# Performance work log

Hardware: AMD Instinct MI355X
Metric: run time of the kernel (lower is better)

The kernel has to match this reference:

```python
import jax, jax.numpy as jnp
import numpy as np

SEQ_LEN = 12
BATCH = 2048
IN_DIM = 512
HIDDEN = 1024


def setup_inputs() -> dict:
    key = jax.random.key(0)
    k1, k2, k3, k4 = jax.random.split(key, 4)
    scale = 1.0 / np.sqrt(IN_DIM + HIDDEN)
    return {
        "x": jax.random.normal(k1, (BATCH, SEQ_LEN, IN_DIM), dtype=jnp.float32),
        "coded_cords": jax.random.normal(k2, (BATCH, HIDDEN), dtype=jnp.float32),
        # TF GRUCell fused gate kernel: [in+hidden, 2*hidden] (reset, update), bias init 1.0
        "gate_kernel": jax.random.normal(k3, (IN_DIM + HIDDEN, 2 * HIDDEN), dtype=jnp.float32) * scale,
        "gate_bias": jnp.ones((2 * HIDDEN,), dtype=jnp.float32),
        # candidate kernel: [in+hidden, hidden], zero bias
        "cand_kernel": jax.random.normal(k4, (IN_DIM + HIDDEN, HIDDEN), dtype=jnp.float32) * scale,
        "cand_bias": jnp.zeros((HIDDEN,), dtype=jnp.float32),
    }


def reference(x, coded_cords, gate_kernel, gate_bias, cand_kernel, cand_bias):
    # GRU recurrence (tf.contrib.rnn.GRUCell math), initial state = coded_cords.
    def step(h, xt):
        # xt: [B, D], h: [B, H]
        gates = jax.nn.sigmoid(jnp.concatenate([xt, h], axis=-1) @ gate_kernel + gate_bias)
        r, u = jnp.split(gates, 2, axis=-1)  # reset, update gates [B, H]
        c = jnp.tanh(jnp.concatenate([xt, r * h], axis=-1) @ cand_kernel + cand_bias)
        h_new = u * h + (1.0 - u) * c
        return h_new, h_new

    xs = jnp.swapaxes(x, 0, 1)  # [T, B, D]
    _, ys = jax.lax.scan(step, coded_cords, xs)  # ys: [T, B, H]
    return jnp.swapaxes(ys, 0, 1)  # [B, T, H]
```

## Files before the change

kernel.cpp:

```cpp
#include <hip/hip_runtime.h>
#include <hip/hip_bf16.h>


#define T_SEQ 12
#define BATCH 2048
#define IND 512
#define HID 1024
#define NGATE (2 * HID)
#define NPRE (NGATE + HID)

typedef __bf16 bf16x8 __attribute__((ext_vector_type(8)));
typedef __bf16 bf16x4 __attribute__((ext_vector_type(4)));
typedef float floatx4 __attribute__((ext_vector_type(4)));

#define AS1 __attribute__((address_space(1)))
#define AS3 __attribute__((address_space(3)))

__device__ __forceinline__ void gload16(const __bf16* g, __bf16* l) {
  __builtin_amdgcn_global_load_lds((const AS1 void*)g, (AS3 void*)l, 16, 0, 0);
}
__device__ __forceinline__ void gload16c(const __bf16* g, __bf16* l) {
  __builtin_amdgcn_global_load_lds((const AS1 void*)g, (AS3 void*)l, 16, 0, 1);
}

__device__ __forceinline__ float fast_sigmoid(float v) {
  v = fminf(30.f, fmaxf(-30.f, v));
  return 1.f / (1.f + __expf(-v));
}
__device__ __forceinline__ float fast_tanh(float v) {
  v = fminf(15.f, fmaxf(-15.f, v));
  float e = __expf(2.f * v);
  return (e - 1.f) / (e + 1.f);
}

__global__ __launch_bounds__(256) void prep(
    const float* __restrict__ Wg, const float* __restrict__ Wc,
    const float* __restrict__ x, const float* __restrict__ coded,
    __bf16* __restrict__ Bx, __bf16* __restrict__ Bhg, __bf16* __restrict__ Bhc,
    __bf16* __restrict__ xb, float* __restrict__ h32, __bf16* __restrict__ hb,
    unsigned* __restrict__ ctr) {
  int b = blockIdx.x;
  if (b < 2304) {
    int gid = b * 256 + threadIdx.x;
    int g = gid >> 6, lane = gid & 63;
    const float* W; int ld, row0, ksteps, wid; __bf16* out;
    if (g < 2048)      { W = Wg; ld = NGATE; row0 = 0;   ksteps = 16; wid = g;        out = Bx; }
    else if (g < 3072) { W = Wc; ld = HID;   row0 = 0;   ksteps = 16; wid = g - 2048; out = Bx + (size_t)2048 * 512; }
    else if (g < 7168) { W = Wg; ld = NGATE; row0 = IND; ksteps = 32; wid = g - 3072; out = Bhg; }
    else               { W = Wc; ld = HID;   row0 = IND; ksteps = 32; wid = g - 7168; out = Bhc; }
    int n16 = wid / ksteps, kt = wid - n16 * ksteps;
    int col = n16 * 16 + (lane & 15);
    int k0 = row0 + kt * 32 + (lane >> 4) * 8;
    bf16x8 v;
#pragma unroll
    for (int j = 0; j < 8; ++j) v[j] = (__bf16)W[(size_t)(k0 + j) * ld + col];
    *reinterpret_cast<bf16x8*>(out + (size_t)wid * 512 + lane * 8) = v;
  } else if (b < 4352) {
    int i = (b - 2304) * 256 + threadIdx.x;
    const float4* x4 = (const float4*)x;
    const int n4 = BATCH * T_SEQ * IND / 4;
    for (int k = i; k < n4; k += 2048 * 256) {
      float4 v = x4[k];
      bf16x4 o;
      o[0] = (__bf16)v.x; o[1] = (__bf16)v.y; o[2] = (__bf16)v.z; o[3] = (__bf16)v.w;
      *reinterpret_cast<bf16x4*>(xb + (size_t)k * 4) = o;
    }
  } else {
    int i = (b - 4352) * 256 + threadIdx.x;
    if (b == 4352) {
#pragma unroll
      for (int j = 0; j < 4; ++j) ctr[threadIdx.x + j * 256] = 0u;
    }
    float4 v = ((const float4*)coded)[i];
    ((float4*)h32)[i] = v;
    bf16x4 o;
    o[0] = (__bf16)v.x; o[1] = (__bf16)v.y; o[2] = (__bf16)v.z; o[3] = (__bf16)v.w;
    *reinterpret_cast<bf16x4*>(hb + (size_t)i * 4) = o;
  }
}

__global__ __launch_bounds__(256) void pre_gemm(
    const __bf16* __restrict__ xb, const __bf16* __restrict__ Bx,
    const float* __restrict__ bg, const float* __restrict__ bc,
    __bf16* __restrict__ Pg, __bf16* __restrict__ Pc) {
  __shared__ __bf16 Alds[128 * 64];
  __shared__ __bf16 Blds[8192];
  const int tid = threadIdx.x, lane = tid & 63, w = tid >> 6;
  const int wm = w >> 1, wn = w & 1, quad = lane >> 4, l16 = lane & 15;
  const int bid = blockIdx.x;
  const int wg = (bid & 7) * 576 + (bid >> 3);
  const int nb = wg % 24;
  const int rest = wg / 24;
  const int mB = rest & 15;
  const int tz = rest >> 4;
  const int m0 = mB * 128;

  const __bf16* gA[4]; __bf16* lA[4];
  const __bf16* gB[4]; __bf16* lB[4];
#pragma unroll
  for (int i = 0; i < 4; ++i) {
    int c = tid + i * 256;
    int row = c >> 3, k8 = c & 7;
    gA[i] = xb + ((size_t)(m0 + row) * T_SEQ + tz) * IND + ((k8 ^ (row & 7)) * 8);
    lA[i] = Alds + c * 8;
    int ks2c = c >> 9, rem = c & 511;
    gB[i] = Bx + (((size_t)(nb * 8 + (rem >> 6)) * 16 + ks2c) * 64 + (rem & 63)) * 8;
    lB[i] = Blds + c * 8;
  }

  floatx4 acc[4][4] = {};
  for (int it = 0; it < 8; ++it) {
    __syncthreads();
#pragma unroll
    for (int i = 0; i < 4; ++i) gload16(gA[i] + it * 64, lA[i]);
#pragma unroll
    for (int i = 0; i < 4; ++i) gload16(gB[i] + (size_t)it * 1024, lB[i]);
    __syncthreads();
#pragma unroll
    for (int ks2 = 0; ks2 < 2; ++ks2) {
      bf16x8 af[4], bfr[4];
#pragma unroll
      for (int mf = 0; mf < 4; ++mf) {
        int row = wm * 64 + mf * 16 + l16;
        af[mf] = *(const bf16x8*)&Alds[row * 64 + (((ks2 * 4 + quad) ^ (row & 7)) * 8)];
      }
#pragma unroll
      for (int nf = 0; nf < 4; ++nf)
        bfr[nf] = *(const bf16x8*)&Blds[(ks2 * 512 + (wn * 4 + nf) * 64 + lane) * 8];
#pragma unroll
      for (int mf = 0; mf < 4; ++mf)
#pragma unroll
        for (int nf = 0; nf < 4; ++nf)
          acc[mf][nf] = __builtin_amdgcn_mfma_f32_16x16x32_bf16(af[mf], bfr[nf], acc[mf][nf], 0, 0, 0);
    }
  }

  const int n64g = nb * 2 + wn;
  const bool isg = (n64g < 32);
  __bf16* P = isg ? Pg : Pc;
  const float* bias = isg ? bg : bc;
  const int nrel = isg ? n64g : (n64g - 32);
  const int colb = nrel * 64 + l16;
#pragma unroll
  for (int mf = 0; mf < 4; ++mf) {
    int m32 = mB * 4 + wm * 2 + (mf >> 1);
    size_t tb = isg ? (((size_t)tz * 64 + m32) * 32 + n64g) * 2048
                    : (((size_t)tz * 64 + m32) * 16 + nrel) * 2048;
#pragma unroll
    for (int nf = 0; nf < 4; ++nf) {
      float bv = bias[colb + nf * 16];
      bf16x4 st;
#pragma unroll
      for (int i = 0; i < 4; ++i) st[i] = (__bf16)(acc[mf][nf][i] + bv);
      *(bf16x4*)&P[tb + (size_t)(((mf & 1) * 4 + nf) * 64 + lane) * 4] = st;
    }
  }
}

__global__ __launch_bounds__(256, 2) void gru_steps(
    const __bf16* __restrict__ Bhg, const __bf16* __restrict__ Bhc,
    const __bf16* __restrict__ Pg, const __bf16* __restrict__ Pc,
    float* __restrict__ h32, __bf16* __restrict__ hb,
    __bf16* __restrict__ rhb, float* __restrict__ out,
    unsigned* __restrict__ ctr) {
  __shared__ __bf16 Alds[64 * 128];
  __shared__ __bf16 Blds[16384];
  float* uS = (float*)&Blds[8192];
  const int tid = threadIdx.x, lane = tid & 63, w = tid >> 6;
  const int wm = w >> 1, wn = w & 1, quad = lane >> 4, l16 = lane & 15;
  const int bid = blockIdx.x;
  const int mT = (bid & 7) * 4 + ((bid >> 3) & 3);
  const int sub = bid >> 5;
  unsigned* cG = ctr + mT * 16;
  unsigned* cC = ctr + 512 + mT * 16;

  int offA[4];
#pragma unroll
  for (int i = 0; i < 4; ++i) {
    int c = tid + i * 256, row = c >> 4, ch = c & 15;
    offA[i] = (mT * 64 + row) * HID + ((ch ^ (row & 7)) * 8);
  }

  for (int t = 0; t < T_SEQ; ++t) {
    {
      floatx4 acc[2][4] = {};
      __bf16 hr[2][4][4];
      for (int kt = 0; kt < 8; ++kt) {
        __syncthreads();
#pragma unroll
        for (int i = 0; i < 4; ++i)
          gload16c(hb + offA[i] + kt * 128, Alds + (tid + i * 256) * 8);
#pragma unroll
        for (int i = 0; i < 8; ++i) {
          int gidx = (i < 4) ? (sub * 4 + i) : (64 + sub * 4 + (i - 4));
          gload16(Bhg + (size_t)gidx * 16384 + kt * 2048 + tid * 8,
                  Blds + (tid + i * 256) * 8);
        }
        __syncthreads();
#pragma unroll
        for (int ks2 = 0; ks2 < 4; ++ks2) {
          bf16x8 af[2], bfr[4];
#pragma unroll
          for (int mf = 0; mf < 2; ++mf) {
            int row = wm * 32 + mf * 16 + l16;
            af[mf] = *(const bf16x8*)&Alds[row * 128 + (((ks2 * 4 + quad) ^ (row & 7)) * 8)];
          }
#pragma unroll
          for (int nf = 0; nf < 4; ++nf)
            bfr[nf] = *(const bf16x8*)&Blds[(wn * 4 + nf) * 2048 + ks2 * 512 + lane * 8];
#pragma unroll
          for (int mf = 0; mf < 2; ++mf)
#pragma unroll
            for (int nf = 0; nf < 4; ++nf)
              acc[mf][nf] = __builtin_amdgcn_mfma_f32_16x16x32_bf16(af[mf], bfr[nf], acc[mf][nf], 0, 0, 0);
        }
        if (kt == (sub >> 1) && wn == 0) {
#pragma unroll
          for (int mf = 0; mf < 2; ++mf)
#pragma unroll
            for (int nf = 0; nf < 4; ++nf)
#pragma unroll
              for (int i = 0; i < 4; ++i) {
                int r = wm * 32 + mf * 16 + quad * 4 + i;
                int c = (sub & 1) * 64 + nf * 16 + l16;
                hr[mf][nf][i] = Alds[r * 128 + (((c >> 3) ^ (r & 7)) * 8) + (c & 7)];
              }
        }
      }
      const int n64 = wn * 16 + sub;
      const int m32 = mT * 2 + wm;
      size_t tb = (((size_t)t * 64 + m32) * 32 + n64) * 2048;
#pragma unroll
      for (int mf = 0; mf < 2; ++mf)
#pragma unroll
        for (int nf = 0; nf < 4; ++nf) {
          bf16x4 px = *(const bf16x4*)&Pg[tb + (size_t)((mf * 4 + nf) * 64 + lane) * 4];
          int rowb = mT * 64 + wm * 32 + mf * 16 + quad * 4;
#pragma unroll
          for (int i = 0; i < 4; ++i) {
            float s = fast_sigmoid(acc[mf][nf][i] + (float)px[i]);
            if (wn == 0) {
              rhb[(size_t)(rowb + i) * HID + sub * 64 + nf * 16 + l16] =
                  (__bf16)(s * (float)hr[mf][nf][i]);
            } else {
              uS[(wm * 32 + mf * 16 + quad * 4 + i) * 64 + nf * 16 + l16] = s;
            }
          }
        }
    }
    __syncthreads();
    if (tid == 0) {
      __hip_atomic_fetch_add(cG, 1u, __ATOMIC_RELAXED, __HIP_MEMORY_SCOPE_AGENT);
      unsigned tgt = 16u * (t + 1);
      while (__hip_atomic_load(cG, __ATOMIC_RELAXED, __HIP_MEMORY_SCOPE_AGENT) < tgt)
        __builtin_amdgcn_s_sleep(2);
    }
    __syncthreads();
    {
      floatx4 acc[2][2] = {};
      for (int kt = 0; kt < 8; ++kt) {
        __syncthreads();
#pragma unroll
        for (int i = 0; i < 4; ++i)
          gload16c(rhb + offA[i] + kt * 128, Alds + (tid + i * 256) * 8);
#pragma unroll
        for (int i = 0; i < 4; ++i)
          gload16(Bhc + (size_t)(sub * 4 + i) * 16384 + kt * 2048 + tid * 8,
                  Blds + (tid + i * 256) * 8);
        __syncthreads();
#pragma unroll
        for (int ks2 = 0; ks2 < 4; ++ks2) {
          bf16x8 af[2], bfr[2];
#pragma unroll
          for (int mf = 0; mf < 2; ++mf) {
            int row = wm * 32 + mf * 16 + l16;
            af[mf] = *(const bf16x8*)&Alds[row * 128 + (((ks2 * 4 + quad) ^ (row & 7)) * 8)];
          }
#pragma unroll
          for (int nf = 0; nf < 2; ++nf)
            bfr[nf] = *(const bf16x8*)&Blds[(wn * 2 + nf) * 2048 + ks2 * 512 + lane * 8];
#pragma unroll
          for (int mf = 0; mf < 2; ++mf)
#pragma unroll
            for (int nf = 0; nf < 2; ++nf)
              acc[mf][nf] = __builtin_amdgcn_mfma_f32_16x16x32_bf16(af[mf], bfr[nf], acc[mf][nf], 0, 0, 0);
        }
      }
      const int m32 = mT * 2 + wm;
      size_t tb = (((size_t)t * 64 + m32) * 16 + sub) * 2048;
#pragma unroll
      for (int mf = 0; mf < 2; ++mf)
#pragma unroll
        for (int nf = 0; nf < 2; ++nf) {
          bf16x4 px = *(const bf16x4*)&Pc[tb + (size_t)((mf * 4 + wn * 2 + nf) * 64 + lane) * 4];
          int col = sub * 64 + wn * 32 + nf * 16 + l16;
          int rowb = mT * 64 + wm * 32 + mf * 16 + quad * 4;
#pragma unroll
          for (int i = 0; i < 4; ++i) {
            float c = fast_tanh(acc[mf][nf][i] + (float)px[i]);
            size_t idx = (size_t)(rowb + i) * HID + col;
            float u = uS[(wm * 32 + mf * 16 + quad * 4 + i) * 64 + wn * 32 + nf * 16 + l16];
            float hnew = u * h32[idx] + (1.f - u) * c;
            h32[idx] = hnew;
            hb[idx] = (__bf16)hnew;
            __builtin_nontemporal_store(hnew, &out[(size_t)(rowb + i) * (T_SEQ * HID) + t * HID + col]);
          }
        }
    }
    __syncthreads();
    if (tid == 0) {
      __hip_atomic_fetch_add(cC, 1u, __ATOMIC_RELAXED, __HIP_MEMORY_SCOPE_AGENT);
      unsigned tgt = 16u * (t + 1);
      while (__hip_atomic_load(cC, __ATOMIC_RELAXED, __HIP_MEMORY_SCOPE_AGENT) < tgt)
        __builtin_amdgcn_s_sleep(2);
    }
    __syncthreads();
  }
}

extern "C" void kernel_launch(void* const* d_in, const int* in_sizes, int n_in,
                              void* d_out, int out_size, void* d_ws, size_t ws_size,
                              hipStream_t stream) {
  const float* x     = (const float*)d_in[0];
  const float* coded = (const float*)d_in[1];
  const float* Wg_f  = (const float*)d_in[2];
  const float* bg    = (const float*)d_in[3];
  const float* Wc_f  = (const float*)d_in[4];
  const float* bc    = (const float*)d_in[5];
  float* out = (float*)d_out;

  uintptr_t base = ((uintptr_t)d_ws + 255) & ~(uintptr_t)255;
  auto take = [&](size_t bytes) {
    void* p = (void*)base;
    base = (base + bytes + 255) & ~(uintptr_t)255;
    return p;
  };
  __bf16* Bx  = (__bf16*)take((size_t)(NPRE / 16) * 16 * 512 * 2);
  __bf16* Bhg = (__bf16*)take((size_t)(NGATE / 16) * 32 * 512 * 2);
  __bf16* Bhc = (__bf16*)take((size_t)(HID / 16) * 32 * 512 * 2);
  __bf16* Pg  = (__bf16*)take((size_t)T_SEQ * 64 * 32 * 2048 * 2);
  __bf16* Pc  = (__bf16*)take((size_t)T_SEQ * 64 * 16 * 2048 * 2);
  __bf16* xb  = (__bf16*)take((size_t)BATCH * T_SEQ * IND * 2);
  float*  h32 = (float*) take((size_t)BATCH * HID * 4);
  __bf16* hb  = (__bf16*)take((size_t)BATCH * HID * 2);
  __bf16* rhb = (__bf16*)take((size_t)BATCH * HID * 2);
  unsigned* ctr = (unsigned*)take(1024 * sizeof(unsigned));

  prep<<<6400, 256, 0, stream>>>(Wg_f, Wc_f, x, coded, Bx, Bhg, Bhc, xb, h32, hb, ctr);

  pre_gemm<<<4608, 256, 0, stream>>>(xb, Bx, bg, bc, Pg, Pc);

  gru_steps<<<512, 256, 0, stream>>>(Bhg, Bhc, Pg, Pc, h32, hb, rhb, out, ctr);
}
```

Measured before the change: 716.8 us.

## Fuse input projection GEMM into recurrent GRU step kernel

Removes the separate pre_gemm kernel and its Pg/Pc bf16 buffers. Each step's gate and candidate GEMMs now run four extra K-tiles over the x slice and Bx weights before the hidden-state tiles, and add the biases directly. This saves the large precomputed-projection write and read traffic and one kernel launch. In exchange, the x-projection work moves onto the serial recurrent critical path, which runs with only 512 blocks. It also swizzles the uS shared buffer to avoid bank conflicts and reads h for r*h from global instead of caching it from LDS.

```diff
diff --git a/kernel.cpp b/kernel.cpp
--- a/kernel.cpp
+++ b/kernel.cpp
@@ -79,87 +79,10 @@
   }
 }
 
-__global__ __launch_bounds__(256) void pre_gemm(
-    const __bf16* __restrict__ xb, const __bf16* __restrict__ Bx,
+__global__ __launch_bounds__(256, 2) void gru_steps(
+    const __bf16* __restrict__ Bx, const __bf16* __restrict__ Bhg,
+    const __bf16* __restrict__ Bhc, const __bf16* __restrict__ xb,
     const float* __restrict__ bg, const float* __restrict__ bc,
-    __bf16* __restrict__ Pg, __bf16* __restrict__ Pc) {
-  __shared__ __bf16 Alds[128 * 64];
-  __shared__ __bf16 Blds[8192];
-  const int tid = threadIdx.x, lane = tid & 63, w = tid >> 6;
-  const int wm = w >> 1, wn = w & 1, quad = lane >> 4, l16 = lane & 15;
-  const int bid = blockIdx.x;
-  const int wg = (bid & 7) * 576 + (bid >> 3);
-  const int nb = wg % 24;
-  const int rest = wg / 24;
-  const int mB = rest & 15;
-  const int tz = rest >> 4;
-  const int m0 = mB * 128;
-
-  const __bf16* gA[4]; __bf16* lA[4];
-  const __bf16* gB[4]; __bf16* lB[4];
-#pragma unroll
-  for (int i = 0; i < 4; ++i) {
-    int c = tid + i * 256;
-    int row = c >> 3, k8 = c & 7;
-    gA[i] = xb + ((size_t)(m0 + row) * T_SEQ + tz) * IND + ((k8 ^ (row & 7)) * 8);
-    lA[i] = Alds + c * 8;
-    int ks2c = c >> 9, rem = c & 511;
-    gB[i] = Bx + (((size_t)(nb * 8 + (rem >> 6)) * 16 + ks2c) * 64 + (rem & 63)) * 8;
-    lB[i] = Blds + c * 8;
-  }
-
-  floatx4 acc[4][4] = {};
-  for (int it = 0; it < 8; ++it) {
-    __syncthreads();
-#pragma unroll
-    for (int i = 0; i < 4; ++i) gload16(gA[i] + it * 64, lA[i]);
-#pragma unroll
-    for (int i = 0; i < 4; ++i) gload16(gB[i] + (size_t)it * 1024, lB[i]);
-    __syncthreads();
-#pragma unroll
-    for (int ks2 = 0; ks2 < 2; ++ks2) {
-      bf16x8 af[4], bfr[4];
-#pragma unroll
-      for (int mf = 0; mf < 4; ++mf) {
-        int row = wm * 64 + mf * 16 + l16;
-        af[mf] = *(const bf16x8*)&Alds[row * 64 + (((ks2 * 4 + quad) ^ (row & 7)) * 8)];
-      }
-#pragma unroll
-      for (int nf = 0; nf < 4; ++nf)
-        bfr[nf] = *(const bf16x8*)&Blds[(ks2 * 512 + (wn * 4 + nf) * 64 + lane) * 8];
-#pragma unroll
-      for (int mf = 0; mf < 4; ++mf)
-#pragma unroll
-        for (int nf = 0; nf < 4; ++nf)
-          acc[mf][nf] = __builtin_amdgcn_mfma_f32_16x16x32_bf16(af[mf], bfr[nf], acc[mf][nf], 0, 0, 0);
-    }
-  }
-
-  const int n64g = nb * 2 + wn;
-  const bool isg = (n64g < 32);
-  __bf16* P = isg ? Pg : Pc;
-  const float* bias = isg ? bg : bc;
-  const int nrel = isg ? n64g : (n64g - 32);
-  const int colb = nrel * 64 + l16;
-#pragma unroll
-  for (int mf = 0; mf < 4; ++mf) {
-    int m32 = mB * 4 + wm * 2 + (mf >> 1);
-    size_t tb = isg ? (((size_t)tz * 64 + m32) * 32 + n64g) * 2048
-                    : (((size_t)tz * 64 + m32) * 16 + nrel) * 2048;
-#pragma unroll
-    for (int nf = 0; nf < 4; ++nf) {
-      float bv = bias[colb + nf * 16];
-      bf16x4 st;
-#pragma unroll
-      for (int i = 0; i < 4; ++i) st[i] = (__bf16)(acc[mf][nf][i] + bv);
-      *(bf16x4*)&P[tb + (size_t)(((mf & 1) * 4 + nf) * 64 + lane) * 4] = st;
-    }
-  }
-}
-
-__global__ __launch_bounds__(256, 2) void gru_steps(
-    const __bf16* __restrict__ Bhg, const __bf16* __restrict__ Bhc,
-    const __bf16* __restrict__ Pg, const __bf16* __restrict__ Pc,
     float* __restrict__ h32, __bf16* __restrict__ hb,
     __bf16* __restrict__ rhb, float* __restrict__ out,
     unsigned* __restrict__ ctr) {
@@ -174,27 +97,49 @@
   unsigned* cG = ctr + mT * 16;
   unsigned* cC = ctr + 512 + mT * 16;
 
-  int offA[4];
+  auto uSi = [](int r, int c) { return r * 64 + (c ^ (((r >> 2) & 3) << 4)); };
+
+  int axOff[4], ahOff[4];
 #pragma unroll
   for (int i = 0; i < 4; ++i) {
-    int c = tid + i * 256, row = c >> 4, ch = c & 15;
-    offA[i] = (mT * 64 + row) * HID + ((ch ^ (row & 7)) * 8);
+    int c = tid + i * 256, row = c >> 4, x8 = ((c & 15) ^ (row & 7)) * 8;
+    axOff[i] = (mT * 64 + row) * (T_SEQ * IND) + x8;
+    ahOff[i] = (mT * 64 + row) * HID + x8;
+  }
+  int bgx[8], bgh[8], bcx[4], bch[4];
+#pragma unroll
+  for (int i = 0; i < 8; ++i) {
+    int n16g = (i < 4) ? (sub * 4 + i) : (64 + sub * 4 + (i - 4));
+    bgx[i] = n16g * 8192 + tid * 8;
+    bgh[i] = n16g * 16384 + tid * 8;
+  }
+#pragma unroll
+  for (int i = 0; i < 4; ++i) {
+    int n16c = sub * 4 + i;
+    bcx[i] = 2048 * 512 + n16c * 8192 + tid * 8;
+    bch[i] = n16c * 16384 + tid * 8;
   }
 
   for (int t = 0; t < T_SEQ; ++t) {
+    const int xT = t * 512;
     {
       floatx4 acc[2][4] = {};
-      __bf16 hr[2][4][4];
-      for (int kt = 0; kt < 8; ++kt) {
-        __syncthreads();
-#pragma unroll
-        for (int i = 0; i < 4; ++i)
-          gload16c(hb + offA[i] + kt * 128, Alds + (tid + i * 256) * 8);
-#pragma unroll
-        for (int i = 0; i < 8; ++i) {
-          int gidx = (i < 4) ? (sub * 4 + i) : (64 + sub * 4 + (i - 4));
-          gload16(Bhg + (size_t)gidx * 16384 + kt * 2048 + tid * 8,
-                  Blds + (tid + i * 256) * 8);
+      for (int kt = 0; kt < 12; ++kt) {
+        __syncthreads();
+        if (kt < 4) {
+#pragma unroll
+          for (int i = 0; i < 4; ++i)
+            gload16(xb + axOff[i] + xT + kt * 128, Alds + (tid + i * 256) * 8);
+#pragma unroll
+          for (int i = 0; i < 8; ++i)
+            gload16(Bx + bgx[i] + kt * 2048, Blds + (tid + i * 256) * 8);
+        } else {
+#pragma unroll
+          for (int i = 0; i < 4; ++i)
+            gload16c(hb + ahOff[i] + (kt - 4) * 128, Alds + (tid + i * 256) * 8);
+#pragma unroll
+          for (int i = 0; i < 8; ++i)
+            gload16(Bhg + bgh[i] + (kt - 4) * 2048, Blds + (tid + i * 256) * 8);
         }
         __syncthreads();
 #pragma unroll
@@ -214,39 +159,28 @@
             for (int nf = 0; nf < 4; ++nf)
               acc[mf][nf] = __builtin_amdgcn_mfma_f32_16x16x32_bf16(af[mf], bfr[nf], acc[mf][nf], 0, 0, 0);
         }
-        if (kt == (sub >> 1) && wn == 0) {
-#pragma unroll
-          for (int mf = 0; mf < 2; ++mf)
-#pragma unroll
-            for (int nf = 0; nf < 4; ++nf)
-#pragma unroll
-              for (int i = 0; i < 4; ++i) {
-                int r = wm * 32 + mf * 16 + quad * 4 + i;
-                int c = (sub & 1) * 64 + nf * 16 + l16;
-                hr[mf][nf][i] = Alds[r * 128 + (((c >> 3) ^ (r & 7)) * 8) + (c & 7)];
-              }
-        }
-      }
-      const int n64 = wn * 16 + sub;
-      const int m32 = mT * 2 + wm;
-      size_t tb = (((size_t)t * 64 + m32) * 32 + n64) * 2048;
-#pragma unroll
-      for (int mf = 0; mf < 2; ++mf)
+      }
+      const int colb = (wn * 16 + sub) * 64 + l16;
+      float bgv[4];
+#pragma unroll
+      for (int nf = 0; nf < 4; ++nf) bgv[nf] = bg[colb + nf * 16];
+#pragma unroll
+      for (int mf = 0; mf < 2; ++mf) {
+        int rowb = mT * 64 + wm * 32 + mf * 16 + quad * 4;
 #pragma unroll
         for (int nf = 0; nf < 4; ++nf) {
-          bf16x4 px = *(const bf16x4*)&Pg[tb + (size_t)((mf * 4 + nf) * 64 + lane) * 4];
-          int rowb = mT * 64 + wm * 32 + mf * 16 + quad * 4;
 #pragma unroll
           for (int i = 0; i < 4; ++i) {
-            float s = fast_sigmoid(acc[mf][nf][i] + (float)px[i]);
+            float s = fast_sigmoid(acc[mf][nf][i] + bgv[nf]);
             if (wn == 0) {
-              rhb[(size_t)(rowb + i) * HID + sub * 64 + nf * 16 + l16] =
-                  (__bf16)(s * (float)hr[mf][nf][i]);
+              size_t idx = (size_t)(rowb + i) * HID + sub * 64 + nf * 16 + l16;
+              rhb[idx] = (__bf16)(s * (float)hb[idx]);
             } else {
-              uS[(wm * 32 + mf * 16 + quad * 4 + i) * 64 + nf * 16 + l16] = s;
+              uS[uSi(wm * 32 + mf * 16 + quad * 4 + i, nf * 16 + l16)] = s;
             }
           }
         }
+      }
     }
     __syncthreads();
     if (tid == 0) {
@@ -258,15 +192,23 @@
     __syncthreads();
     {
       floatx4 acc[2][2] = {};
-      for (int kt = 0; kt < 8; ++kt) {
-        __syncthreads();
-#pragma unroll
-        for (int i = 0; i < 4; ++i)
-          gload16c(rhb + offA[i] + kt * 128, Alds + (tid + i * 256) * 8);
-#pragma unroll
-        for (int i = 0; i < 4; ++i)
-          gload16(Bhc + (size_t)(sub * 4 + i) * 16384 + kt * 2048 + tid * 8,
-                  Blds + (tid + i * 256) * 8);
+      for (int kt = 0; kt < 12; ++kt) {
+        __syncthreads();
+        if (kt < 4) {
+#pragma unroll
+          for (int i = 0; i < 4; ++i)
+            gload16(xb + axOff[i] + xT + kt * 128, Alds + (tid + i * 256) * 8);
+#pragma unroll
+          for (int i = 0; i < 4; ++i)
+            gload16(Bx + bcx[i] + kt * 2048, Blds + (tid + i * 256) * 8);
+        } else {
+#pragma unroll
+          for (int i = 0; i < 4; ++i)
+            gload16c(rhb + ahOff[i] + (kt - 4) * 128, Alds + (tid + i * 256) * 8);
+#pragma unroll
+          for (int i = 0; i < 4; ++i)
+            gload16(Bhc + bch[i] + (kt - 4) * 2048, Blds + (tid + i * 256) * 8);
+        }
         __syncthreads();
 #pragma unroll
         for (int ks2 = 0; ks2 < 4; ++ks2) {
@@ -286,26 +228,25 @@
               acc[mf][nf] = __builtin_amdgcn_mfma_f32_16x16x32_bf16(af[mf], bfr[nf], acc[mf][nf], 0, 0, 0);
         }
       }
-      const int m32 = mT * 2 + wm;
-      size_t tb = (((size_t)t * 64 + m32) * 16 + sub) * 2048;
-#pragma unroll
-      for (int mf = 0; mf < 2; ++mf)
+#pragma unroll
+      for (int mf = 0; mf < 2; ++mf) {
 #pragma unroll
         for (int nf = 0; nf < 2; ++nf) {
-          bf16x4 px = *(const bf16x4*)&Pc[tb + (size_t)((mf * 4 + wn * 2 + nf) * 64 + lane) * 4];
           int col = sub * 64 + wn * 32 + nf * 16 + l16;
+          float bcv = bc[col];
           int rowb = mT * 64 + wm * 32 + mf * 16 + quad * 4;
 #pragma unroll
           for (int i = 0; i < 4; ++i) {
-            float c = fast_tanh(acc[mf][nf][i] + (float)px[i]);
+            float c = fast_tanh(acc[mf][nf][i] + bcv);
             size_t idx = (size_t)(rowb + i) * HID + col;
-            float u = uS[(wm * 32 + mf * 16 + quad * 4 + i) * 64 + wn * 32 + nf * 16 + l16];
+            float u = uS[uSi(wm * 32 + mf * 16 + quad * 4 + i, wn * 32 + nf * 16 + l16)];
             float hnew = u * h32[idx] + (1.f - u) * c;
             h32[idx] = hnew;
             hb[idx] = (__bf16)hnew;
             __builtin_nontemporal_store(hnew, &out[(size_t)(rowb + i) * (T_SEQ * HID) + t * HID + col]);
           }
         }
+      }
     }
     __syncthreads();
     if (tid == 0) {
@@ -338,8 +279,6 @@
   __bf16* Bx  = (__bf16*)take((size_t)(NPRE / 16) * 16 * 512 * 2);
   __bf16* Bhg = (__bf16*)take((size_t)(NGATE / 16) * 32 * 512 * 2);
   __bf16* Bhc = (__bf16*)take((size_t)(HID / 16) * 32 * 512 * 2);
-  __bf16* Pg  = (__bf16*)take((size_t)T_SEQ * 64 * 32 * 2048 * 2);
-  __bf16* Pc  = (__bf16*)take((size_t)T_SEQ * 64 * 16 * 2048 * 2);
   __bf16* xb  = (__bf16*)take((size_t)BATCH * T_SEQ * IND * 2);
   float*  h32 = (float*) take((size_t)BATCH * HID * 4);
   __bf16* hb  = (__bf16*)take((size_t)BATCH * HID * 2);
@@ -348,7 +287,5 @@
 
   prep<<<6400, 256, 0, stream>>>(Wg_f, Wc_f, x, coded, Bx, Bhg, Bhc, xb, h32, hb, ctr);
 
-  pre_gemm<<<4608, 256, 0, stream>>>(xb, Bx, bg, bc, Pg, Pc);
-
-  gru_steps<<<512, 256, 0, stream>>>(Bhg, Bhc, Pg, Pc, h32, hb, rhb, out, ctr);
-}
+  gru_steps<<<512, 256, 0, stream>>>(Bx, Bhg, Bhc, xb, bg, bc, h32, hb, rhb, out, ctr);
+}
```

After: 1.097 ms. +53.0%, slower.

## Halve GRU step tile rows and double persistent blocks for more occupancy

Applied to the files above, without the earlier changes.

The recurrent kernel now uses 32-row batch tiles instead of 64, launching 1024 persistent blocks with smaller LDS and a K-tile of 64, so more blocks fit per CU. Each wave now covers all rows and a slice of columns. The reset-gate multiply reads h from the fp32 state instead of caching it from LDS during the GEMM. The uS buffer gets its own swizzled LDS array, and the counter array is enlarged for the extra tiles. This buys more parallelism and latency hiding per step, at the cost of twice as many barrier groups and more redundant weight loads per block. It also relies on all 1024 blocks being co-resident, because of the spin barriers.

```diff
diff --git a/kernel.cpp b/kernel.cpp
--- a/kernel.cpp
+++ b/kernel.cpp
@@ -69,7 +69,7 @@
     int i = (b - 4352) * 256 + threadIdx.x;
     if (b == 4352) {
 #pragma unroll
-      for (int j = 0; j < 4; ++j) ctr[threadIdx.x + j * 256] = 0u;
+      for (int j = 0; j < 8; ++j) ctr[threadIdx.x + j * 256] = 0u;
     }
     float4 v = ((const float4*)coded)[i];
     ((float4*)h32)[i] = v;
@@ -157,96 +157,91 @@
   }
 }
 
-__global__ __launch_bounds__(256, 2) void gru_steps(
+__global__ __launch_bounds__(256, 5) void gru_steps(
     const __bf16* __restrict__ Bhg, const __bf16* __restrict__ Bhc,
     const __bf16* __restrict__ Pg, const __bf16* __restrict__ Pc,
     float* __restrict__ h32, __bf16* __restrict__ hb,
     __bf16* __restrict__ rhb, float* __restrict__ out,
     unsigned* __restrict__ ctr) {
-  __shared__ __bf16 Alds[64 * 128];
-  __shared__ __bf16 Blds[16384];
-  float* uS = (float*)&Blds[8192];
+  __shared__ __bf16 Alds[32 * 64];
+  __shared__ __bf16 Blds[8192];
+  __shared__ float uS[32 * 64];
   const int tid = threadIdx.x, lane = tid & 63, w = tid >> 6;
-  const int wm = w >> 1, wn = w & 1, quad = lane >> 4, l16 = lane & 15;
+  const int quad = lane >> 4, l16 = lane & 15;
   const int bid = blockIdx.x;
-  const int mT = (bid & 7) * 4 + ((bid >> 3) & 3);
-  const int sub = bid >> 5;
+  const int mT = (bid & 7) * 8 + ((bid >> 3) & 7);
+  const int sub = bid >> 6;
   unsigned* cG = ctr + mT * 16;
-  unsigned* cC = ctr + 512 + mT * 16;
-
-  int offA[4];
+  unsigned* cC = ctr + 1024 + mT * 16;
+
+  auto uSi = [](int r, int c) { return r * 64 + (c ^ (((r >> 2) & 3) << 4)); };
+
+  const int arow = tid >> 3;
+  const int ahOff = (mT * 32 + arow) * HID + (((tid & 7) ^ (arow & 7)) * 8);
+  int bghS[4], bchS[2];
 #pragma unroll
   for (int i = 0; i < 4; ++i) {
-    int c = tid + i * 256, row = c >> 4, ch = c & 15;
-    offA[i] = (mT * 64 + row) * HID + ((ch ^ (row & 7)) * 8);
+    int c = tid + i * 256, s = c >> 7;
+    int n16g = (s < 4) ? (sub * 4 + s) : (64 + sub * 4 + (s - 4));
+    bghS[i] = n16g * 16384 + (c & 127) * 8;
+  }
+#pragma unroll
+  for (int i = 0; i < 2; ++i) {
+    int c = tid + i * 256;
+    bchS[i] = (sub * 4 + (c >> 7)) * 16384 + (c & 127) * 8;
   }
 
   for (int t = 0; t < T_SEQ; ++t) {
     {
-      floatx4 acc[2][4] = {};
-      __bf16 hr[2][4][4];
-      for (int kt = 0; kt < 8; ++kt) {
+      floatx4 acc[2][2] = {};
+      for (int kt = 0; kt < 16; ++kt) {
         __syncthreads();
+        gload16c(hb + ahOff + kt * 64, Alds + tid * 8);
 #pragma unroll
         for (int i = 0; i < 4; ++i)
-          gload16c(hb + offA[i] + kt * 128, Alds + (tid + i * 256) * 8);
-#pragma unroll
-        for (int i = 0; i < 8; ++i) {
-          int gidx = (i < 4) ? (sub * 4 + i) : (64 + sub * 4 + (i - 4));
-          gload16(Bhg + (size_t)gidx * 16384 + kt * 2048 + tid * 8,
-                  Blds + (tid + i * 256) * 8);
-        }
+          gload16(Bhg + bghS[i] + kt * 1024, Blds + (tid + i * 256) * 8);
         __syncthreads();
 #pragma unroll
-        for (int ks2 = 0; ks2 < 4; ++ks2) {
-          bf16x8 af[2], bfr[4];
+        for (int ks2 = 0; ks2 < 2; ++ks2) {
+          bf16x8 af[2], bfr[2];
 #pragma unroll
           for (int mf = 0; mf < 2; ++mf) {
-            int row = wm * 32 + mf * 16 + l16;
-            af[mf] = *(const bf16x8*)&Alds[row * 128 + (((ks2 * 4 + quad) ^ (row & 7)) * 8)];
+            int row = mf * 16 + l16;
+            af[mf] = *(const bf16x8*)&Alds[row * 64 + (((ks2 * 4 + quad) ^ (row & 7)) * 8)];
           }
 #pragma unroll
-          for (int nf = 0; nf < 4; ++nf)
-            bfr[nf] = *(const bf16x8*)&Blds[(wn * 4 + nf) * 2048 + ks2 * 512 + lane * 8];
+          for (int nf = 0; nf < 2; ++nf)
+            bfr[nf] = *(const bf16x8*)&Blds[(w * 2 + nf) * 1024 + ks2 * 512 + lane * 8];
 #pragma unroll
           for (int mf = 0; mf < 2; ++mf)
 #pragma unroll
-            for (int nf = 0; nf < 4; ++nf)
+            for (int nf = 0; nf < 2; ++nf)
               acc[mf][nf] = __builtin_amdgcn_mfma_f32_16x16x32_bf16(af[mf], bfr[nf], acc[mf][nf], 0, 0, 0);
         }
-        if (kt == (sub >> 1) && wn == 0) {
-#pragma unroll
-          for (int mf = 0; mf < 2; ++mf)
-#pragma unroll
-            for (int nf = 0; nf < 4; ++nf)
-#pragma unroll
-              for (int i = 0; i < 4; ++i) {
-                int r = wm * 32 + mf * 16 + quad * 4 + i;
-                int c = (sub & 1) * 64 + nf * 16 + l16;
-                hr[mf][nf][i] = Alds[r * 128 + (((c >> 3) ^ (r & 7)) * 8) + (c & 7)];
-              }
-        }
-      }
-      const int n64 = wn * 16 + sub;
-      const int m32 = mT * 2 + wm;
-      size_t tb = (((size_t)t * 64 + m32) * 32 + n64) * 2048;
-#pragma unroll
-      for (int mf = 0; mf < 2; ++mf)
-#pragma unroll
-        for (int nf = 0; nf < 4; ++nf) {
-          bf16x4 px = *(const bf16x4*)&Pg[tb + (size_t)((mf * 4 + nf) * 64 + lane) * 4];
-          int rowb = mT * 64 + wm * 32 + mf * 16 + quad * 4;
+      }
+      const bool isr = (w < 2);
+      const int n64 = isr ? sub : (16 + sub);
+      size_t tb = (((size_t)t * 64 + mT) * 32 + n64) * 2048;
+#pragma unroll
+      for (int mf = 0; mf < 2; ++mf) {
+        int rowb = mT * 32 + mf * 16 + quad * 4;
+#pragma unroll
+        for (int nf = 0; nf < 2; ++nf) {
+          bf16x4 px = *(const bf16x4*)&Pg[tb + (size_t)((mf * 4 + (w & 1) * 2 + nf) * 64 + lane) * 4];
+          int cl = (w & 1) * 32 + nf * 16 + l16;
 #pragma unroll
           for (int i = 0; i < 4; ++i) {
             float s = fast_sigmoid(acc[mf][nf][i] + (float)px[i]);
-            if (wn == 0) {
-              rhb[(size_t)(rowb + i) * HID + sub * 64 + nf * 16 + l16] =
-                  (__bf16)(s * (float)hr[mf][nf][i]);
+            if (isr) {
+              size_t idx = (size_t)(rowb + i) * HID + sub * 64 + cl;
+              float hv = (float)(__bf16)h32[idx];
+              rhb[idx] = (__bf16)(s * hv);
             } else {
-              uS[(wm * 32 + mf * 16 + quad * 4 + i) * 64 + nf * 16 + l16] = s;
+              uS[uSi(mf * 16 + quad * 4 + i, cl)] = s;
             }
           }
         }
+      }
     }
     __syncthreads();
     if (tid == 0) {
@@ -257,55 +252,45 @@
     }
     __syncthreads();
     {
-      floatx4 acc[2][2] = {};
-      for (int kt = 0; kt < 8; ++kt) {
+      floatx4 acc2[2] = {};
+      for (int kt = 0; kt < 16; ++kt) {
         __syncthreads();
-#pragma unroll
-        for (int i = 0; i < 4; ++i)
-          gload16c(rhb + offA[i] + kt * 128, Alds + (tid + i * 256) * 8);
-#pragma unroll
-        for (int i = 0; i < 4; ++i)
-          gload16(Bhc + (size_t)(sub * 4 + i) * 16384 + kt * 2048 + tid * 8,
-                  Blds + (tid + i * 256) * 8);
+        gload16c(rhb + ahOff + kt * 64, Alds + tid * 8);
+#pragma unroll
+        for (int i = 0; i < 2; ++i)
+          gload16(Bhc + bchS[i] + kt * 1024, Blds + (tid + i * 256) * 8);
         __syncthreads();
 #pragma unroll
-        for (int ks2 = 0; ks2 < 4; ++ks2) {
-          bf16x8 af[2], bfr[2];
+        for (int ks2 = 0; ks2 < 2; ++ks2) {
+          bf16x8 af[2], bfr;
 #pragma unroll
           for (int mf = 0; mf < 2; ++mf) {
-            int row = wm * 32 + mf * 16 + l16;
-            af[mf] = *(const bf16x8*)&Alds[row * 128 + (((ks2 * 4 + quad) ^ (row & 7)) * 8)];
+            int row = mf * 16 + l16;
+            af[mf] = *(const bf16x8*)&Alds[row * 64 + (((ks2 * 4 + quad) ^ (row & 7)) * 8)];
           }
-#pragma unroll
-          for (int nf = 0; nf < 2; ++nf)
-            bfr[nf] = *(const bf16x8*)&Blds[(wn * 2 + nf) * 2048 + ks2 * 512 + lane * 8];
+          bfr = *(const bf16x8*)&Blds[w * 1024 + ks2 * 512 + lane * 8];
 #pragma unroll
           for (int mf = 0; mf < 2; ++mf)
-#pragma unroll
-            for (int nf = 0; nf < 2; ++nf)
-              acc[mf][nf] = __builtin_amdgcn_mfma_f32_16x16x32_bf16(af[mf], bfr[nf], acc[mf][nf], 0, 0, 0);
+            acc2[mf] = __builtin_amdgcn_mfma_f32_16x16x32_bf16(af[mf], bfr, acc2[mf], 0, 0, 0);
         }
       }
-      const int m32 = mT * 2 + wm;
-      size_t tb = (((size_t)t * 64 + m32) * 16 + sub) * 2048;
-#pragma unroll
-      for (int mf = 0; mf < 2; ++mf)
-#pragma unroll
-        for (int nf = 0; nf < 2; ++nf) {
-          bf16x4 px = *(const bf16x4*)&Pc[tb + (size_t)((mf * 4 + wn * 2 + nf) * 64 + lane) * 4];
-          int col = sub * 64 + wn * 32 + nf * 16 + l16;
-          int rowb = mT * 64 + wm * 32 + mf * 16 + quad * 4;
-#pragma unroll
-          for (int i = 0; i < 4; ++i) {
-            float c = fast_tanh(acc[mf][nf][i] + (float)px[i]);
-            size_t idx = (size_t)(rowb + i) * HID + col;
-            float u = uS[(wm * 32 + mf * 16 + quad * 4 + i) * 64 + wn * 32 + nf * 16 + l16];
-            float hnew = u * h32[idx] + (1.f - u) * c;
-            h32[idx] = hnew;
-            hb[idx] = (__bf16)hnew;
-            __builtin_nontemporal_store(hnew, &out[(size_t)(rowb + i) * (T_SEQ * HID) + t * HID + col]);
-          }
+      size_t tb = (((size_t)t * 64 + mT) * 16 + sub) * 2048;
+#pragma unroll
+      for (int mf = 0; mf < 2; ++mf) {
+        bf16x4 px = *(const bf16x4*)&Pc[tb + (size_t)((mf * 4 + w) * 64 + lane) * 4];
+        int col = sub * 64 + w * 16 + l16;
+        int rowb = mT * 32 + mf * 16 + quad * 4;
+#pragma unroll
+        for (int i = 0; i < 4; ++i) {
+          float c = fast_tanh(acc2[mf][i] + (float)px[i]);
+          size_t idx = (size_t)(rowb + i) * HID + col;
+          float u = uS[uSi(mf * 16 + quad * 4 + i, w * 16 + l16)];
+          float hnew = u * h32[idx] + (1.f - u) * c;
+          h32[idx] = hnew;
+          hb[idx] = (__bf16)hnew;
+          __builtin_nontemporal_store(hnew, &out[(size_t)(rowb + i) * (T_SEQ * HID) + t * HID + col]);
         }
+      }
     }
     __syncthreads();
     if (tid == 0) {
@@ -344,11 +329,11 @@
   float*  h32 = (float*) take((size_t)BATCH * HID * 4);
   __bf16* hb  = (__bf16*)take((size_t)BATCH * HID * 2);
   __bf16* rhb = (__bf16*)take((size_t)BATCH * HID * 2);
-  unsigned* ctr = (unsigned*)take(1024 * sizeof(unsigned));
+  unsigned* ctr = (unsigned*)take(2048 * sizeof(unsigned));
 
   prep<<<6400, 256, 0, stream>>>(Wg_f, Wc_f, x, coded, Bx, Bhg, Bhc, xb, h32, hb, ctr);
 
   pre_gemm<<<4608, 256, 0, stream>>>(xb, Bx, bg, bc, Pg, Pc);
 
-  gru_steps<<<512, 256, 0, stream>>>(Bhg, Bhc, Pg, Pc, h32, hb, rhb, out, ctr);
-}
+  gru_steps<<<1024, 256, 0, stream>>>(Bhg, Bhc, Pg, Pc, h32, hb, rhb, out, ctr);
+}
```

Result: slower. 1.149 ms (+60.3%).

## Double-buffer LDS tiles in GRU step GEMMs with halved K-tile

Applied to the files above, without the earlier changes.

Both recurrent GEMM phases in gru_steps now use two LDS buffers with a 64-wide K tile over 16 iterations. Loads for the next tile are issued before computing the current one, so there is one barrier per iteration instead of two. The reset-gate product now reads h from global h32, rounded to bf16, instead of capturing it from LDS. The update gate is stored as fp16 in a swizzled LDS region. This aims to hide global-to-LDS latency behind MFMA work, at the cost of extra global reads of h and twice as many loop iterations.

```diff
diff --git a/kernel.cpp b/kernel.cpp
--- a/kernel.cpp
+++ b/kernel.cpp
@@ -69,7 +69,7 @@
     int i = (b - 4352) * 256 + threadIdx.x;
     if (b == 4352) {
 #pragma unroll
-      for (int j = 0; j < 4; ++j) ctr[threadIdx.x + j * 256] = 0u;
+      for (int j = 0; j < 8; ++j) ctr[threadIdx.x + j * 256] = 0u;
     }
     float4 v = ((const float4*)coded)[i];
     ((float4*)h32)[i] = v;
@@ -163,9 +163,9 @@
     float* __restrict__ h32, __bf16* __restrict__ hb,
     __bf16* __restrict__ rhb, float* __restrict__ out,
     unsigned* __restrict__ ctr) {
-  __shared__ __bf16 Alds[64 * 128];
+  __shared__ __bf16 Alds[2][4096];
   __shared__ __bf16 Blds[16384];
-  float* uS = (float*)&Blds[8192];
+  _Float16* uS = (_Float16*)&Blds[12288];
   const int tid = threadIdx.x, lane = tid & 63, w = tid >> 6;
   const int wm = w >> 1, wn = w & 1, quad = lane >> 4, l16 = lane & 15;
   const int bid = blockIdx.x;
@@ -174,79 +174,87 @@
   unsigned* cG = ctr + mT * 16;
   unsigned* cC = ctr + 512 + mT * 16;
 
-  int offA[4];
+  auto uSi = [](int r, int c) { return r * 64 + (c ^ (((r >> 2) & 3) << 4)); };
+
+  int ahOff[2];
+#pragma unroll
+  for (int i = 0; i < 2; ++i) {
+    int c = tid + i * 256, row = c >> 3;
+    ahOff[i] = (mT * 64 + row) * HID + (((c & 7) ^ (row & 7)) * 8);
+  }
+  int bghS[4];
 #pragma unroll
   for (int i = 0; i < 4; ++i) {
-    int c = tid + i * 256, row = c >> 4, ch = c & 15;
-    offA[i] = (mT * 64 + row) * HID + ((ch ^ (row & 7)) * 8);
+    int c = tid + i * 256, s = c >> 7;
+    int n16g = (s < 4) ? (sub * 4 + s) : (64 + sub * 4 + (s - 4));
+    bghS[i] = n16g * 16384 + (c & 127) * 8;
+  }
+  int bchS[2];
+#pragma unroll
+  for (int i = 0; i < 2; ++i) {
+    int c = tid + i * 256;
+    bchS[i] = (sub * 4 + (c >> 7)) * 16384 + (c & 127) * 8;
   }
 
   for (int t = 0; t < T_SEQ; ++t) {
     {
       floatx4 acc[2][4] = {};
-      __bf16 hr[2][4][4];
-      for (int kt = 0; kt < 8; ++kt) {
-        __syncthreads();
-#pragma unroll
-        for (int i = 0; i < 4; ++i)
-          gload16c(hb + offA[i] + kt * 128, Alds + (tid + i * 256) * 8);
-#pragma unroll
-        for (int i = 0; i < 8; ++i) {
-          int gidx = (i < 4) ? (sub * 4 + i) : (64 + sub * 4 + (i - 4));
-          gload16(Bhg + (size_t)gidx * 16384 + kt * 2048 + tid * 8,
-                  Blds + (tid + i * 256) * 8);
-        }
-        __syncthreads();
-#pragma unroll
-        for (int ks2 = 0; ks2 < 4; ++ks2) {
+#pragma unroll
+      for (int i = 0; i < 2; ++i) gload16c(hb + ahOff[i], Alds[0] + (tid + i * 256) * 8);
+#pragma unroll
+      for (int i = 0; i < 4; ++i) gload16(Bhg + bghS[i], Blds + (tid + i * 256) * 8);
+      __syncthreads();
+      for (int kt = 0; kt < 16; ++kt) {
+        const int cur = kt & 1;
+        if (kt + 1 < 16) {
+#pragma unroll
+          for (int i = 0; i < 2; ++i)
+            gload16c(hb + ahOff[i] + (kt + 1) * 64, Alds[cur ^ 1] + (tid + i * 256) * 8);
+#pragma unroll
+          for (int i = 0; i < 4; ++i)
+            gload16(Bhg + bghS[i] + (kt + 1) * 1024, Blds + (cur ^ 1) * 8192 + (tid + i * 256) * 8);
+        }
+#pragma unroll
+        for (int ks2 = 0; ks2 < 2; ++ks2) {
           bf16x8 af[2], bfr[4];
 #pragma unroll
           for (int mf = 0; mf < 2; ++mf) {
             int row = wm * 32 + mf * 16 + l16;
-            af[mf] = *(const bf16x8*)&Alds[row * 128 + (((ks2 * 4 + quad) ^ (row & 7)) * 8)];
+            af[mf] = *(const bf16x8*)&Alds[cur][row * 64 + (((ks2 * 4 + quad) ^ (row & 7)) * 8)];
           }
 #pragma unroll
           for (int nf = 0; nf < 4; ++nf)
-            bfr[nf] = *(const bf16x8*)&Blds[(wn * 4 + nf) * 2048 + ks2 * 512 + lane * 8];
+            bfr[nf] = *(const bf16x8*)&Blds[cur * 8192 + (wn * 4 + nf) * 1024 + ks2 * 512 + lane * 8];
 #pragma unroll
           for (int mf = 0; mf < 2; ++mf)
 #pragma unroll
             for (int nf = 0; nf < 4; ++nf)
               acc[mf][nf] = __builtin_amdgcn_mfma_f32_16x16x32_bf16(af[mf], bfr[nf], acc[mf][nf], 0, 0, 0);
         }
-        if (kt == (sub >> 1) && wn == 0) {
-#pragma unroll
-          for (int mf = 0; mf < 2; ++mf)
-#pragma unroll
-            for (int nf = 0; nf < 4; ++nf)
-#pragma unroll
-              for (int i = 0; i < 4; ++i) {
-                int r = wm * 32 + mf * 16 + quad * 4 + i;
-                int c = (sub & 1) * 64 + nf * 16 + l16;
-                hr[mf][nf][i] = Alds[r * 128 + (((c >> 3) ^ (r & 7)) * 8) + (c & 7)];
-              }
-        }
+        __syncthreads();
       }
       const int n64 = wn * 16 + sub;
       const int m32 = mT * 2 + wm;
       size_t tb = (((size_t)t * 64 + m32) * 32 + n64) * 2048;
 #pragma unroll
-      for (int mf = 0; mf < 2; ++mf)
+      for (int mf = 0; mf < 2; ++mf) {
+        int rowb = mT * 64 + wm * 32 + mf * 16 + quad * 4;
 #pragma unroll
         for (int nf = 0; nf < 4; ++nf) {
           bf16x4 px = *(const bf16x4*)&Pg[tb + (size_t)((mf * 4 + nf) * 64 + lane) * 4];
-          int rowb = mT * 64 + wm * 32 + mf * 16 + quad * 4;
 #pragma unroll
           for (int i = 0; i < 4; ++i) {
             float s = fast_sigmoid(acc[mf][nf][i] + (float)px[i]);
             if (wn == 0) {
-              rhb[(size_t)(rowb + i) * HID + sub * 64 + nf * 16 + l16] =
-                  (__bf16)(s * (float)hr[mf][nf][i]);
+              size_t idx = (size_t)(rowb + i) * HID + sub * 64 + nf * 16 + l16;
+              float hv = (float)(__bf16)h32[idx];
+              rhb[idx] = (__bf16)(s * hv);
             } else {
-              uS[(wm * 32 + mf * 16 + quad * 4 + i) * 64 + nf * 16 + l16] = s;
+              uS[uSi(wm * 32 + mf * 16 + quad * 4 + i, nf * 16 + l16)] = (_Float16)s;
             }
           }
         }
+      }
     }
     __syncthreads();
     if (tid == 0) {
@@ -258,38 +266,44 @@
     __syncthreads();
     {
       floatx4 acc[2][2] = {};
-      for (int kt = 0; kt < 8; ++kt) {
-        __syncthreads();
-#pragma unroll
-        for (int i = 0; i < 4; ++i)
-          gload16c(rhb + offA[i] + kt * 128, Alds + (tid + i * 256) * 8);
-#pragma unroll
-        for (int i = 0; i < 4; ++i)
-          gload16(Bhc + (size_t)(sub * 4 + i) * 16384 + kt * 2048 + tid * 8,
-                  Blds + (tid + i * 256) * 8);
-        __syncthreads();
-#pragma unroll
-        for (int ks2 = 0; ks2 < 4; ++ks2) {
+#pragma unroll
+      for (int i = 0; i < 2; ++i) gload16c(rhb + ahOff[i], Alds[0] + (tid + i * 256) * 8);
+#pragma unroll
+      for (int i = 0; i < 2; ++i) gload16(Bhc + bchS[i], Blds + (tid + i * 256) * 8);
+      __syncthreads();
+      for (int kt = 0; kt < 16; ++kt) {
+        const int cur = kt & 1;
+        if (kt + 1 < 16) {
+#pragma unroll
+          for (int i = 0; i < 2; ++i)
+            gload16c(rhb + ahOff[i] + (kt + 1) * 64, Alds[cur ^ 1] + (tid + i * 256) * 8);
+#pragma unroll
+          for (int i = 0; i < 2; ++i)
+            gload16(Bhc + bchS[i] + (kt + 1) * 1024, Blds + (cur ^ 1) * 4096 + (tid + i * 256) * 8);
+        }
+#pragma unroll
+        for (int ks2 = 0; ks2 < 2; ++ks2) {
           bf16x8 af[2], bfr[2];
 #pragma unroll
           for (int mf = 0; mf < 2; ++mf) {
             int row = wm * 32 + mf * 16 + l16;
-            af[mf] = *(const bf16x8*)&Alds[row * 128 + (((ks2 * 4 + quad) ^ (row & 7)) * 8)];
+            af[mf] = *(const bf16x8*)&Alds[cur][row * 64 + (((ks2 * 4 + quad) ^ (row & 7)) * 8)];
           }
 #pragma unroll
           for (int nf = 0; nf < 2; ++nf)
-            bfr[nf] = *(const bf16x8*)&Blds[(wn * 2 + nf) * 2048 + ks2 * 512 + lane * 8];
+            bfr[nf] = *(const bf16x8*)&Blds[cur * 4096 + (wn * 2 + nf) * 1024 + ks2 * 512 + lane * 8];
 #pragma unroll
           for (int mf = 0; mf < 2; ++mf)
 #pragma unroll
             for (int nf = 0; nf < 2; ++nf)
               acc[mf][nf] = __builtin_amdgcn_mfma_f32_16x16x32_bf16(af[mf], bfr[nf], acc[mf][nf], 0, 0, 0);
         }
+        __syncthreads();
       }
       const int m32 = mT * 2 + wm;
       size_t tb = (((size_t)t * 64 + m32) * 16 + sub) * 2048;
 #pragma unroll
-      for (int mf = 0; mf < 2; ++mf)
+      for (int mf = 0; mf < 2; ++mf) {
 #pragma unroll
         for (int nf = 0; nf < 2; ++nf) {
           bf16x4 px = *(const bf16x4*)&Pc[tb + (size_t)((mf * 4 + wn * 2 + nf) * 64 + lane) * 4];
@@ -299,13 +313,14 @@
           for (int i = 0; i < 4; ++i) {
             float c = fast_tanh(acc[mf][nf][i] + (float)px[i]);
             size_t idx = (size_t)(rowb + i) * HID + col;
-            float u = uS[(wm * 32 + mf * 16 + quad * 4 + i) * 64 + wn * 32 + nf * 16 + l16];
+            float u = (float)uS[uSi(wm * 32 + mf * 16 + quad * 4 + i, wn * 32 + nf * 16 + l16)];
             float hnew = u * h32[idx] + (1.f - u) * c;
             h32[idx] = hnew;
             hb[idx] = (__bf16)hnew;
             __builtin_nontemporal_store(hnew, &out[(size_t)(rowb + i) * (T_SEQ * HID) + t * HID + col]);
           }
         }
+      }
     }
     __syncthreads();
     if (tid == 0) {
@@ -344,7 +359,7 @@
   float*  h32 = (float*) take((size_t)BATCH * HID * 4);
   __bf16* hb  = (__bf16*)take((size_t)BATCH * HID * 2);
   __bf16* rhb = (__bf16*)take((size_t)BATCH * HID * 2);
-  unsigned* ctr = (unsigned*)take(1024 * sizeof(unsigned));
+  unsigned* ctr = (unsigned*)take(2048 * sizeof(unsigned));
 
   prep<<<6400, 256, 0, stream>>>(Wg_f, Wc_f, x, coded, Bx, Bhg, Bhc, xb, h32, hb, ctr);
 
```

Result: slower. 1.291 ms (+80.2%).
